# Optimization experiments

Hardware: AMD Instinct MI355X
Metric: run time of the kernel (lower is better)

The kernel has to match this reference:

```python
import jax, jax.numpy as jnp
import numpy as np

SEQ, BATCH, IN_DIM, HID_DIM = 512, 256, 256, 256
NQ = 8
ALPHA = 0.5
MLP_HID = 128


def _linear_init(key, fan_in, fan_out):
    k1, k2 = jax.random.split(key)
    bound = 1.0 / np.sqrt(fan_in)
    W = jax.random.uniform(k1, (fan_in, fan_out), minval=-bound, maxval=bound, dtype=jnp.float32)
    b = jax.random.uniform(k2, (fan_out,), minval=-bound, maxval=bound, dtype=jnp.float32)
    return W, b


def setup_inputs() -> dict:
    key = jax.random.key(0)
    ks = jax.random.split(key, 12)
    cdim = IN_DIM + HID_DIM
    inputs = jax.random.normal(ks[0], (SEQ, BATCH, IN_DIM), dtype=jnp.float32)
    W1, b1 = _linear_init(ks[1], cdim, MLP_HID)
    W2, b2 = _linear_init(ks[2], MLP_HID, NQ * 4)
    Wf, bf = _linear_init(ks[3], cdim, 1)
    Wi, bi = _linear_init(ks[4], cdim, 1)
    Wg, bg = _linear_init(ks[5], cdim, 1)
    Wo, bo = _linear_init(ks[6], cdim, 1)
    rzf = jax.random.normal(ks[7], (NQ,), dtype=jnp.float32)
    rzi = jax.random.normal(ks[8], (NQ,), dtype=jnp.float32)
    rzg = jax.random.normal(ks[9], (NQ,), dtype=jnp.float32)
    rzo = jax.random.normal(ks[10], (NQ,), dtype=jnp.float32)
    return dict(inputs=inputs, W1=W1, b1=b1, W2=W2, b2=b2,
                Wf=Wf, bf=bf, Wi=Wi, bi=bi, Wg=Wg, bg=bg, Wo=Wo, bo=bo,
                rzf=rzf, rzi=rzi, rzg=rzg, rzo=rzo)


def _qgate(theta):
    # Analytic expectations of the RX/RZ/CNOT-chain circuit:
    # <Z_k> = prod_{j<=k} cos(theta_j); rz_params cancel in Z expectations.
    # Returns mean over wires, shape (batch, 1).
    return jnp.mean(jnp.cumprod(jnp.cos(theta), axis=-1), axis=-1, keepdims=True)


def reference(inputs, W1, b1, W2, b2, Wf, bf, Wi, bi, Wg, bg, Wo, bo, rzf, rzi, rzg, rzo):
    batch = inputs.shape[1]
    hx0 = jnp.zeros((batch, HID_DIM), dtype=inputs.dtype)
    cx0 = jnp.zeros((batch, HID_DIM), dtype=inputs.dtype)

    def step(carry, x):
        hx, cx = carry
        combined = jnp.concatenate([x, hx], axis=1)  # (B, in+hid)
        f_c = jax.nn.sigmoid(combined @ Wf + bf)
        i_c = jax.nn.sigmoid(combined @ Wi + bi)
        g_c = jnp.tanh(combined @ Wg + bg)
        o_c = jax.nn.sigmoid(combined @ Wo + bo)
        h1 = jax.nn.relu(combined @ W1 + b1)
        q = h1 @ W2 + b2  # (B, 4*NQ)
        q_f = _qgate(q[:, 0 * NQ:1 * NQ])
        q_i = _qgate(q[:, 1 * NQ:2 * NQ])
        q_g = _qgate(q[:, 2 * NQ:3 * NQ])
        q_o = _qgate(q[:, 3 * NQ:4 * NQ])
        f = (1 - ALPHA) * f_c + ALPHA * jax.nn.sigmoid(q_f)
        i = (1 - ALPHA) * i_c + ALPHA * jax.nn.sigmoid(q_i)
        g = (1 - ALPHA) * g_c + ALPHA * jnp.tanh(q_g)
        o = (1 - ALPHA) * o_c + ALPHA * jax.nn.sigmoid(q_o)
        cx_new = f * cx + i * g
        hx_new = o * jnp.tanh(cx_new)
        return (hx_new, cx_new), hx_new

    (hx, cx), outputs = jax.lax.scan(step, (hx0, cx0), inputs)
    return outputs, (hx, cx)
```

## Files before the change

### kernel.cpp

```cpp
#include <hip/hip_runtime.h>

#define SEQ 512
#define BATCH 256
#define INDIM 256
#define MLP 128
#define M_ROWS (SEQ * BATCH)
#define PRE_STRIDE 136
#define AUX_OFF ((size_t)M_ROWS * PRE_STRIDE)

__global__ __launch_bounds__(256) void prep_kernel(
    const float* __restrict__ W1,
    const float* __restrict__ Wf, const float* __restrict__ Wi,
    const float* __restrict__ Wg, const float* __restrict__ Wo,
    const float* __restrict__ bf, const float* __restrict__ bi,
    const float* __restrict__ bg, const float* __restrict__ bo,
    float* __restrict__ aux) {
  const int tid = threadIdx.x;
  if (tid < 128) {
    float s = 0.f;
    for (int k = 0; k < 256; ++k) s += W1[(size_t)(256 + k) * 128 + tid];
    aux[tid] = s;
  } else if (tid < 132) {
    const int g = tid - 128;
    const float* w = (g == 0) ? Wf : (g == 1) ? Wi : (g == 2) ? Wg : Wo;
    float s = 0.f;
    for (int k = 0; k < 256; ++k) s += w[256 + k];
    aux[128 + g] = s;
  } else if (tid < 136) {
    const int g = tid - 132;
    const float* bp = (g == 0) ? bf : (g == 1) ? bi : (g == 2) ? bg : bo;
    aux[132 + g] = bp[0];
  }
}

#define BK 16
#define LDX 132

__global__ __launch_bounds__(256) void gemm_kernel(
    const float* __restrict__ X,
    const float* __restrict__ W1,
    const float* __restrict__ b1p,
    const float* __restrict__ Wf, const float* __restrict__ Wi,
    const float* __restrict__ Wg, const float* __restrict__ Wo,
    const float* __restrict__ bfp, const float* __restrict__ bip,
    const float* __restrict__ bgp, const float* __restrict__ bop,
    float* __restrict__ PRE) {
  __shared__ __align__(16) float Xs[BK * LDX];
  __shared__ __align__(16) float Ws[BK * LDX];
  __shared__ float Wgs[BK * 4];

  const int tid = threadIdx.x;
  const int blk = blockIdx.x;
  const int tx = tid & 15, ty = tid >> 4;
  const int r_st = tid >> 1, kh = (tid & 1) * 8;
  const int wk = tid >> 4, wn = (tid & 15) * 8;
  const int r2 = tid >> 1, gp = (tid & 1) * 2;

  const size_t rowbase = (size_t)blk * 128;

  float acc[8][8] = {};
  float ga = 0.f, gb = 0.f;

  for (int kc = 0; kc < 256; kc += BK) {
    const float4 xa = *(const float4*)&X[(rowbase + r_st) * 256 + kc + kh];
    const float4 xb = *(const float4*)&X[(rowbase + r_st) * 256 + kc + kh + 4];
    const float4 wa = *(const float4*)&W1[(size_t)(kc + wk) * 128 + wn];
    const float4 wb = *(const float4*)&W1[(size_t)(kc + wk) * 128 + wn + 4];
    float wgv = 0.f;
    if (tid < 64) {
      const int kk = tid >> 2, g = tid & 3;
      const float* w = (g == 0) ? Wf : (g == 1) ? Wi : (g == 2) ? Wg : Wo;
      wgv = w[kc + kk];
    }
    __syncthreads();
    Xs[(kh + 0) * LDX + r_st] = xa.x;
    Xs[(kh + 1) * LDX + r_st] = xa.y;
    Xs[(kh + 2) * LDX + r_st] = xa.z;
    Xs[(kh + 3) * LDX + r_st] = xa.w;
    Xs[(kh + 4) * LDX + r_st] = xb.x;
    Xs[(kh + 5) * LDX + r_st] = xb.y;
    Xs[(kh + 6) * LDX + r_st] = xb.z;
    Xs[(kh + 7) * LDX + r_st] = xb.w;
    *(float4*)&Ws[wk * LDX + wn] = wa;
    *(float4*)&Ws[wk * LDX + wn + 4] = wb;
    if (tid < 64) Wgs[tid] = wgv;
    __syncthreads();

#pragma unroll
    for (int kk = 0; kk < BK; ++kk) {
      const float4 a0 = *(const float4*)&Xs[kk * LDX + ty * 8];
      const float4 a1 = *(const float4*)&Xs[kk * LDX + ty * 8 + 4];
      const float4 c0 = *(const float4*)&Ws[kk * LDX + tx * 8];
      const float4 c1 = *(const float4*)&Ws[kk * LDX + tx * 8 + 4];
      const float av[8] = {a0.x, a0.y, a0.z, a0.w, a1.x, a1.y, a1.z, a1.w};
      const float bv[8] = {c0.x, c0.y, c0.z, c0.w, c1.x, c1.y, c1.z, c1.w};
#pragma unroll
      for (int i = 0; i < 8; ++i)
#pragma unroll
        for (int j = 0; j < 8; ++j)
          acc[i][j] = fmaf(av[i], bv[j], acc[i][j]);
      const float xv = Xs[kk * LDX + r2];
      ga = fmaf(xv, Wgs[kk * 4 + gp], ga);
      gb = fmaf(xv, Wgs[kk * 4 + gp + 1], gb);
    }
  }

  float bias[8];
  {
    const float4 u0 = *(const float4*)&b1p[tx * 8];
    const float4 u1 = *(const float4*)&b1p[tx * 8 + 4];
    bias[0] = u0.x; bias[1] = u0.y; bias[2] = u0.z; bias[3] = u0.w;
    bias[4] = u1.x; bias[5] = u1.y; bias[6] = u1.z; bias[7] = u1.w;
  }
#pragma unroll
  for (int i = 0; i < 8; ++i) {
    const size_t row = rowbase + ty * 8 + i;
    float4 o0, o1;
    o0.x = acc[i][0] + bias[0]; o0.y = acc[i][1] + bias[1];
    o0.z = acc[i][2] + bias[2]; o0.w = acc[i][3] + bias[3];
    o1.x = acc[i][4] + bias[4]; o1.y = acc[i][5] + bias[5];
    o1.z = acc[i][6] + bias[6]; o1.w = acc[i][7] + bias[7];
    *(float4*)&PRE[row * PRE_STRIDE + tx * 8] = o0;
    *(float4*)&PRE[row * PRE_STRIDE + tx * 8 + 4] = o1;
  }
  {
    const float ab = (gp == 0) ? bfp[0] : bgp[0];
    const float bb2 = (gp == 0) ? bip[0] : bop[0];
    float2 og;
    og.x = ga + ab; og.y = gb + bb2;
    *(float2*)&PRE[(rowbase + r2) * PRE_STRIDE + 128 + gp] = og;
  }
}

__device__ __forceinline__ float sigmoid_f(float x) {
  return __fdividef(1.0f, 1.0f + __expf(-x));
}
__device__ __forceinline__ float tanh_f(float x) {
  const float e = __expf(-2.0f * x);
  return __fdividef(1.0f - e, 1.0f + e);
}
__device__ __forceinline__ float readlane_f(float v, int lane) {
  return __int_as_float(__builtin_amdgcn_readlane(__float_as_int(v), lane));
}

__global__ __attribute__((amdgpu_waves_per_eu(1, 1))) __launch_bounds__(64)
void rec_kernel(
    const float* __restrict__ PRE, const float* __restrict__ W2,
    const float* __restrict__ b2, const float* __restrict__ aux,
    float* __restrict__ out) {
  __shared__ __align__(16) float h1s[128];

  const int l = threadIdx.x;
  const int b = blockIdx.x;
  const int m = l & 31, half = l >> 5;
  const int g = m >> 3;
  const int g8 = g * 8;

  float w2r[64];
#pragma unroll
  for (int u = 0; u < 64; ++u) w2r[u] = W2[(size_t)(half * 64 + u) * 32 + m];
  const float4 b2a = *(const float4*)&b2[g8];
  const float4 b2b = *(const float4*)&b2[g8 + 4];
  const float2 s1 = *(const float2*)&aux[2 * l];
  const float4 sg = *(const float4*)&aux[128];

  float h = 0.f, c = 0.f;

  const float* pr0 = PRE + (size_t)b * PRE_STRIDE;
  const size_t ts = (size_t)BATCH * PRE_STRIDE;

  float2 p0 = *(const float2*)(pr0 + 0 * ts + 2 * l);
  float4 g0 = *(const float4*)(pr0 + 0 * ts + 128);
  float2 p1 = *(const float2*)(pr0 + 1 * ts + 2 * l);
  float4 g1 = *(const float4*)(pr0 + 1 * ts + 128);

  const float4* h1p = (const float4*)&h1s[half * 64];

  for (int t = 0; t < SEQ; ++t) {
    const float h10 = fmaxf(fmaf(h, s1.x, p0.x), 0.f);
    const float h11 = fmaxf(fmaf(h, s1.y, p0.y), 0.f);

    ((float2*)h1s)[l] = make_float2(h10, h11);
    asm volatile("" ::: "memory");

    const float zf = fmaf(h, sg.x, g0.x);
    const float zi = fmaf(h, sg.y, g0.y);
    const float zg = fmaf(h, sg.z, g0.z);
    const float zo = fmaf(h, sg.w, g0.w);
    const float cf = sigmoid_f(zf);
    const float ci = sigmoid_f(zi);
    const float cg = tanh_f(zg);
    const float co = sigmoid_f(zo);
    p0 = p1; g0 = g1;
    const int tn = (t + 2 < SEQ) ? (t + 2) : (SEQ - 1);
    p1 = *(const float2*)(pr0 + (size_t)tn * ts + 2 * l);
    g1 = *(const float4*)(pr0 + (size_t)tn * ts + 128);

    float q0 = 0.f, q1 = 0.f, q2 = 0.f, q3 = 0.f;
#pragma unroll
    for (int jj = 0; jj < 16; ++jj) {
      const float4 hv = h1p[jj];
      q0 = fmaf(hv.x, w2r[4 * jj + 0], q0);
      q1 = fmaf(hv.y, w2r[4 * jj + 1], q1);
      q2 = fmaf(hv.z, w2r[4 * jj + 2], q2);
      q3 = fmaf(hv.w, w2r[4 * jj + 3], q3);
    }
    const float part = (q0 + q1) + (q2 + q3);

    const float a0 = __shfl(part, g8 + 0, 64), b0 = __shfl(part, 32 + g8 + 0, 64);
    const float a1 = __shfl(part, g8 + 1, 64), b1 = __shfl(part, 32 + g8 + 1, 64);
    const float a2 = __shfl(part, g8 + 2, 64), b2s = __shfl(part, 32 + g8 + 2, 64);
    const float a3 = __shfl(part, g8 + 3, 64), b3 = __shfl(part, 32 + g8 + 3, 64);
    const float a4 = __shfl(part, g8 + 4, 64), b4 = __shfl(part, 32 + g8 + 4, 64);
    const float a5 = __shfl(part, g8 + 5, 64), b5 = __shfl(part, 32 + g8 + 5, 64);
    const float a6 = __shfl(part, g8 + 6, 64), b6 = __shfl(part, 32 + g8 + 6, 64);
    const float a7 = __shfl(part, g8 + 7, 64), b7 = __shfl(part, 32 + g8 + 7, 64);

    const float e0 = __cosf(a0 + b0 + b2a.x);
    const float e1 = __cosf(a1 + b1 + b2a.y);
    const float e2 = __cosf(a2 + b2s + b2a.z);
    const float e3 = __cosf(a3 + b3 + b2a.w);
    const float e4 = __cosf(a4 + b4 + b2b.x);
    const float e5 = __cosf(a5 + b5 + b2b.y);
    const float e6 = __cosf(a6 + b6 + b2b.z);
    const float e7 = __cosf(a7 + b7 + b2b.w);
    float p = e0, s = e0;
    p *= e1; s += p;
    p *= e2; s += p;
    p *= e3; s += p;
    p *= e4; s += p;
    p *= e5; s += p;
    p *= e6; s += p;
    p *= e7; s += p;
    const float qv = s * 0.125f;

    const float qarg = (g == 2) ? (2.0f * qv) : qv;
    const float qs = sigmoid_f(qarg);
    const float av = (g == 2) ? (2.0f * qs - 1.0f) : qs;

    const float aF = readlane_f(av, 0);
    const float aI = readlane_f(av, 8);
    const float aG = readlane_f(av, 16);
    const float aO = readlane_f(av, 24);

    const float f  = 0.5f * (cf + aF);
    const float ii = 0.5f * (ci + aI);
    const float gg = 0.5f * (cg + aG);
    const float oo = 0.5f * (co + aO);

    c = fmaf(f, c, ii * gg);
    h = oo * tanh_f(c);

    float4 hv4o; hv4o.x = h; hv4o.y = h; hv4o.z = h; hv4o.w = h;
    *(float4*)(out + ((size_t)t * BATCH + b) * 256 + 4 * l) = hv4o;
  }

  float4 hq; hq.x = h; hq.y = h; hq.z = h; hq.w = h;
  float4 cq; cq.x = c; cq.y = c; cq.z = c; cq.w = c;
  *(float4*)(out + (size_t)SEQ * BATCH * 256 + (size_t)b * 256 + 4 * l) = hq;
  *(float4*)(out + (size_t)SEQ * BATCH * 256 + (size_t)BATCH * 256 +
             (size_t)b * 256 + 4 * l) = cq;
}

extern "C" void kernel_launch(void* const* d_in, const int* in_sizes, int n_in,
                              void* d_out, int out_size, void* d_ws,
                              size_t ws_size, hipStream_t stream) {
  const float* X  = (const float*)d_in[0];
  const float* W1 = (const float*)d_in[1];
  const float* b1 = (const float*)d_in[2];
  const float* W2 = (const float*)d_in[3];
  const float* b2 = (const float*)d_in[4];
  const float* Wf = (const float*)d_in[5];
  const float* bf = (const float*)d_in[6];
  const float* Wi = (const float*)d_in[7];
  const float* bi = (const float*)d_in[8];
  const float* Wg = (const float*)d_in[9];
  const float* bg = (const float*)d_in[10];
  const float* Wo = (const float*)d_in[11];
  const float* bo = (const float*)d_in[12];

  float* ws  = (float*)d_ws;
  float* PRE = ws;
  float* aux = ws + AUX_OFF;
  float* out = (float*)d_out;

  prep_kernel<<<1, 256, 0, stream>>>(W1, Wf, Wi, Wg, Wo, bf, bi, bg, bo, aux);
  gemm_kernel<<<M_ROWS / 128, 256, 0, stream>>>(X, W1, b1, Wf, Wi, Wg, Wo,
                                                bf, bi, bg, bo, PRE);
  rec_kernel<<<BATCH, 64, 0, stream>>>(PRE, W2, b2, aux, out);
}
```

Before: 762.1 us.

## Use bf16 MFMA for input projection and interleave two batch rows per recurrent wave

The fp32 SIMT GEMM that projects the inputs onto the MLP and gate weights is replaced by a bf16 MFMA 16x16x32 GEMM. A new prep kernel transposes and converts the weights to bf16, and the activations are rounded to bf16 on load. Separately, the recurrent kernel now processes two batch rows per 64-lane wave, interleaving their independent dependency chains to hide latency while halving the number of workgroups. Using bf16 lowers the precision of the pre-activations, and putting two rows on each wave halves the parallelism across CUs.

```diff
diff --git a/kernel.cpp b/kernel.cpp
--- a/kernel.cpp
+++ b/kernel.cpp
@@ -8,8 +8,16 @@
 #define PRE_STRIDE 136
 #define AUX_OFF ((size_t)M_ROWS * PRE_STRIDE)
 
+typedef __attribute__((ext_vector_type(8))) short short8v;
+typedef __attribute__((ext_vector_type(4))) float f32x4;
+
+__device__ __forceinline__ ushort bf16_rne(float x) {
+  const uint u = __float_as_uint(x);
+  return (ushort)((u + 0x7FFFu + ((u >> 16) & 1u)) >> 16);
+}
+
 __global__ __launch_bounds__(256) void prep_kernel(
-    const float* __restrict__ W1,
+    const float* __restrict__ W1, const float* __restrict__ b1p,
     const float* __restrict__ Wf, const float* __restrict__ Wi,
     const float* __restrict__ Wg, const float* __restrict__ Wo,
     const float* __restrict__ bf, const float* __restrict__ bi,
@@ -26,109 +34,96 @@
     float s = 0.f;
     for (int k = 0; k < 256; ++k) s += w[256 + k];
     aux[128 + g] = s;
-  } else if (tid < 136) {
-    const int g = tid - 132;
-    const float* bp = (g == 0) ? bf : (g == 1) ? bi : (g == 2) ? bg : bo;
-    aux[132 + g] = bp[0];
-  }
-}
-
-#define BK 16
-#define LDX 132
-
-__global__ __launch_bounds__(256) void gemm_kernel(
-    const float* __restrict__ X,
+  }
+  if (tid < 144) {
+    float v;
+    if (tid < 128) v = b1p[tid];
+    else if (tid < 132) {
+      const int g = tid - 128;
+      v = (g == 0) ? bf[0] : (g == 1) ? bi[0] : (g == 2) ? bg[0] : bo[0];
+    } else v = 0.f;
+    aux[160 + tid] = v;
+  }
+}
+
+__global__ __launch_bounds__(256) void prep2_kernel(
     const float* __restrict__ W1,
-    const float* __restrict__ b1p,
     const float* __restrict__ Wf, const float* __restrict__ Wi,
     const float* __restrict__ Wg, const float* __restrict__ Wo,
-    const float* __restrict__ bfp, const float* __restrict__ bip,
-    const float* __restrict__ bgp, const float* __restrict__ bop,
-    float* __restrict__ PRE) {
-  __shared__ __align__(16) float Xs[BK * LDX];
-  __shared__ __align__(16) float Ws[BK * LDX];
-  __shared__ float Wgs[BK * 4];
+    ushort* __restrict__ W1T) {
+  const int n = blockIdx.x;
+  const int k = threadIdx.x;
+  float v;
+  if (n < 128) v = W1[(size_t)k * 128 + n];
+  else if (n < 132) {
+    const int g = n - 128;
+    const float* w = (g == 0) ? Wf : (g == 1) ? Wi : (g == 2) ? Wg : Wo;
+    v = w[k];
+  } else v = 0.f;
+  W1T[(size_t)n * 264 + k] = bf16_rne(v);
+}
+
+__global__ __launch_bounds__(256) void gemm_kernel(
+    const float* __restrict__ X, const ushort* __restrict__ W1T,
+    const float* __restrict__ b1ext, float* __restrict__ PRE) {
+  __shared__ __align__(16) ushort As[64 * 40];
+  __shared__ __align__(16) ushort Bs[144 * 40];
 
   const int tid = threadIdx.x;
-  const int blk = blockIdx.x;
-  const int tx = tid & 15, ty = tid >> 4;
-  const int r_st = tid >> 1, kh = (tid & 1) * 8;
-  const int wk = tid >> 4, wn = (tid & 15) * 8;
-  const int r2 = tid >> 1, gp = (tid & 1) * 2;
-
-  const size_t rowbase = (size_t)blk * 128;
-
-  float acc[8][8] = {};
-  float ga = 0.f, gb = 0.f;
-
-  for (int kc = 0; kc < 256; kc += BK) {
-    const float4 xa = *(const float4*)&X[(rowbase + r_st) * 256 + kc + kh];
-    const float4 xb = *(const float4*)&X[(rowbase + r_st) * 256 + kc + kh + 4];
-    const float4 wa = *(const float4*)&W1[(size_t)(kc + wk) * 128 + wn];
-    const float4 wb = *(const float4*)&W1[(size_t)(kc + wk) * 128 + wn + 4];
-    float wgv = 0.f;
-    if (tid < 64) {
-      const int kk = tid >> 2, g = tid & 3;
-      const float* w = (g == 0) ? Wf : (g == 1) ? Wi : (g == 2) ? Wg : Wo;
-      wgv = w[kc + kk];
-    }
+  const int lane = tid & 63, wave = tid >> 6;
+  const int m = lane & 15, quad = lane >> 4;
+  const int arow = tid >> 2, aseg = tid & 3;
+  const size_t rowbase = (size_t)blockIdx.x * 64;
+
+  const f32x4 zero = {0.f, 0.f, 0.f, 0.f};
+  f32x4 acc[9];
+#pragma unroll
+  for (int nt = 0; nt < 9; ++nt) acc[nt] = zero;
+
+  for (int kc = 0; kc < 256; kc += 32) {
     __syncthreads();
-    Xs[(kh + 0) * LDX + r_st] = xa.x;
-    Xs[(kh + 1) * LDX + r_st] = xa.y;
-    Xs[(kh + 2) * LDX + r_st] = xa.z;
-    Xs[(kh + 3) * LDX + r_st] = xa.w;
-    Xs[(kh + 4) * LDX + r_st] = xb.x;
-    Xs[(kh + 5) * LDX + r_st] = xb.y;
-    Xs[(kh + 6) * LDX + r_st] = xb.z;
-    Xs[(kh + 7) * LDX + r_st] = xb.w;
-    *(float4*)&Ws[wk * LDX + wn] = wa;
-    *(float4*)&Ws[wk * LDX + wn + 4] = wb;
-    if (tid < 64) Wgs[tid] = wgv;
+    {
+      const float* src = &X[(rowbase + arow) * 256 + kc + aseg * 8];
+      const float4 v0 = *(const float4*)src;
+      const float4 v1 = *(const float4*)(src + 4);
+      uint4 w;
+      w.x = (uint)bf16_rne(v0.x) | ((uint)bf16_rne(v0.y) << 16);
+      w.y = (uint)bf16_rne(v0.z) | ((uint)bf16_rne(v0.w) << 16);
+      w.z = (uint)bf16_rne(v1.x) | ((uint)bf16_rne(v1.y) << 16);
+      w.w = (uint)bf16_rne(v1.z) | ((uint)bf16_rne(v1.w) << 16);
+      *(uint4*)&As[arow * 40 + aseg * 8] = w;
+    }
+    if (tid < 144) {
+      const ushort* src = &W1T[(size_t)tid * 264 + kc];
+      const uint4 b0 = *(const uint4*)(src + 0);
+      const uint4 b1v = *(const uint4*)(src + 8);
+      const uint4 b2v = *(const uint4*)(src + 16);
+      const uint4 b3v = *(const uint4*)(src + 24);
+      *(uint4*)&Bs[tid * 40 + 0] = b0;
+      *(uint4*)&Bs[tid * 40 + 8] = b1v;
+      *(uint4*)&Bs[tid * 40 + 16] = b2v;
+      *(uint4*)&Bs[tid * 40 + 24] = b3v;
+    }
     __syncthreads();
 
-#pragma unroll
-    for (int kk = 0; kk < BK; ++kk) {
-      const float4 a0 = *(const float4*)&Xs[kk * LDX + ty * 8];
-      const float4 a1 = *(const float4*)&Xs[kk * LDX + ty * 8 + 4];
-      const float4 c0 = *(const float4*)&Ws[kk * LDX + tx * 8];
-      const float4 c1 = *(const float4*)&Ws[kk * LDX + tx * 8 + 4];
-      const float av[8] = {a0.x, a0.y, a0.z, a0.w, a1.x, a1.y, a1.z, a1.w};
-      const float bv[8] = {c0.x, c0.y, c0.z, c0.w, c1.x, c1.y, c1.z, c1.w};
-#pragma unroll
-      for (int i = 0; i < 8; ++i)
-#pragma unroll
-        for (int j = 0; j < 8; ++j)
-          acc[i][j] = fmaf(av[i], bv[j], acc[i][j]);
-      const float xv = Xs[kk * LDX + r2];
-      ga = fmaf(xv, Wgs[kk * 4 + gp], ga);
-      gb = fmaf(xv, Wgs[kk * 4 + gp + 1], gb);
-    }
-  }
-
-  float bias[8];
-  {
-    const float4 u0 = *(const float4*)&b1p[tx * 8];
-    const float4 u1 = *(const float4*)&b1p[tx * 8 + 4];
-    bias[0] = u0.x; bias[1] = u0.y; bias[2] = u0.z; bias[3] = u0.w;
-    bias[4] = u1.x; bias[5] = u1.y; bias[6] = u1.z; bias[7] = u1.w;
-  }
-#pragma unroll
-  for (int i = 0; i < 8; ++i) {
-    const size_t row = rowbase + ty * 8 + i;
-    float4 o0, o1;
-    o0.x = acc[i][0] + bias[0]; o0.y = acc[i][1] + bias[1];
-    o0.z = acc[i][2] + bias[2]; o0.w = acc[i][3] + bias[3];
-    o1.x = acc[i][4] + bias[4]; o1.y = acc[i][5] + bias[5];
-    o1.z = acc[i][6] + bias[6]; o1.w = acc[i][7] + bias[7];
-    *(float4*)&PRE[row * PRE_STRIDE + tx * 8] = o0;
-    *(float4*)&PRE[row * PRE_STRIDE + tx * 8 + 4] = o1;
-  }
-  {
-    const float ab = (gp == 0) ? bfp[0] : bgp[0];
-    const float bb2 = (gp == 0) ? bip[0] : bop[0];
-    float2 og;
-    og.x = ga + ab; og.y = gb + bb2;
-    *(float2*)&PRE[(rowbase + r2) * PRE_STRIDE + 128 + gp] = og;
+    const short8v af = *(const short8v*)&As[(wave * 16 + m) * 40 + quad * 8];
+#pragma unroll
+    for (int nt = 0; nt < 9; ++nt) {
+      const short8v bfr = *(const short8v*)&Bs[(nt * 16 + m) * 40 + quad * 8];
+      acc[nt] = __builtin_amdgcn_mfma_f32_16x16x32_bf16(af, bfr, acc[nt], 0, 0, 0);
+    }
+  }
+
+#pragma unroll
+  for (int nt = 0; nt < 9; ++nt) {
+    const int col = nt * 16 + m;
+    if (col < 132) {
+      const float bias = b1ext[col];
+      const size_t r0 = rowbase + wave * 16 + quad * 4;
+#pragma unroll
+      for (int reg = 0; reg < 4; ++reg)
+        PRE[(r0 + reg) * PRE_STRIDE + col] = acc[nt][reg] + bias;
+    }
   }
 }
 
@@ -148,13 +143,13 @@
     const float* __restrict__ PRE, const float* __restrict__ W2,
     const float* __restrict__ b2, const float* __restrict__ aux,
     float* __restrict__ out) {
-  __shared__ __align__(16) float h1s[128];
+  __shared__ __align__(16) float h1sA[128];
+  __shared__ __align__(16) float h1sB[128];
 
   const int l = threadIdx.x;
-  const int b = blockIdx.x;
   const int m = l & 31, half = l >> 5;
-  const int g = m >> 3;
-  const int g8 = g * 8;
+  const int g = m >> 3, g8 = g * 8;
+  const int bA = blockIdx.x * 2, bB = bA + 1;
 
   float w2r[64];
 #pragma unroll
@@ -164,102 +159,160 @@
   const float2 s1 = *(const float2*)&aux[2 * l];
   const float4 sg = *(const float4*)&aux[128];
 
-  float h = 0.f, c = 0.f;
-
-  const float* pr0 = PRE + (size_t)b * PRE_STRIDE;
+  float hA = 0.f, cA = 0.f, hB = 0.f, cB = 0.f;
+
+  const float* prA = PRE + (size_t)bA * PRE_STRIDE;
+  const float* prB = PRE + (size_t)bB * PRE_STRIDE;
   const size_t ts = (size_t)BATCH * PRE_STRIDE;
 
-  float2 p0 = *(const float2*)(pr0 + 0 * ts + 2 * l);
-  float4 g0 = *(const float4*)(pr0 + 0 * ts + 128);
-  float2 p1 = *(const float2*)(pr0 + 1 * ts + 2 * l);
-  float4 g1 = *(const float4*)(pr0 + 1 * ts + 128);
-
-  const float4* h1p = (const float4*)&h1s[half * 64];
+  float2 pA0 = *(const float2*)(prA + 0 * ts + 2 * l);
+  float4 gA0 = *(const float4*)(prA + 0 * ts + 128);
+  float2 pA1 = *(const float2*)(prA + 1 * ts + 2 * l);
+  float4 gA1 = *(const float4*)(prA + 1 * ts + 128);
+  float2 pB0 = *(const float2*)(prB + 0 * ts + 2 * l);
+  float4 gB0 = *(const float4*)(prB + 0 * ts + 128);
+  float2 pB1 = *(const float2*)(prB + 1 * ts + 2 * l);
+  float4 gB1 = *(const float4*)(prB + 1 * ts + 128);
+
+  const float4* hpA = (const float4*)&h1sA[half * 64];
+  const float4* hpB = (const float4*)&h1sB[half * 64];
 
   for (int t = 0; t < SEQ; ++t) {
-    const float h10 = fmaxf(fmaf(h, s1.x, p0.x), 0.f);
-    const float h11 = fmaxf(fmaf(h, s1.y, p0.y), 0.f);
-
-    ((float2*)h1s)[l] = make_float2(h10, h11);
+    const int tn = (t + 2 < SEQ) ? (t + 2) : (SEQ - 1);
+
+    const float h10A = fmaxf(fmaf(hA, s1.x, pA0.x), 0.f);
+    const float h11A = fmaxf(fmaf(hA, s1.y, pA0.y), 0.f);
+    ((float2*)h1sA)[l] = make_float2(h10A, h11A);
+    const float cfA = sigmoid_f(fmaf(hA, sg.x, gA0.x));
+    const float ciA = sigmoid_f(fmaf(hA, sg.y, gA0.y));
+    const float cgA = tanh_f(fmaf(hA, sg.z, gA0.z));
+    const float coA = sigmoid_f(fmaf(hA, sg.w, gA0.w));
+    pA0 = pA1; gA0 = gA1;
+    pA1 = *(const float2*)(prA + (size_t)tn * ts + 2 * l);
+    gA1 = *(const float4*)(prA + (size_t)tn * ts + 128);
+
+    const float h10B = fmaxf(fmaf(hB, s1.x, pB0.x), 0.f);
+    const float h11B = fmaxf(fmaf(hB, s1.y, pB0.y), 0.f);
+    ((float2*)h1sB)[l] = make_float2(h10B, h11B);
+    const float cfB = sigmoid_f(fmaf(hB, sg.x, gB0.x));
+    const float ciB = sigmoid_f(fmaf(hB, sg.y, gB0.y));
+    const float cgB = tanh_f(fmaf(hB, sg.z, gB0.z));
+    const float coB = sigmoid_f(fmaf(hB, sg.w, gB0.w));
+    pB0 = pB1; gB0 = gB1;
+    pB1 = *(const float2*)(prB + (size_t)tn * ts + 2 * l);
+    gB1 = *(const float4*)(prB + (size_t)tn * ts + 128);
+
     asm volatile("" ::: "memory");
 
-    const float zf = fmaf(h, sg.x, g0.x);
-    const float zi = fmaf(h, sg.y, g0.y);
-    const float zg = fmaf(h, sg.z, g0.z);
-    const float zo = fmaf(h, sg.w, g0.w);
-    const float cf = sigmoid_f(zf);
-    const float ci = sigmoid_f(zi);
-    const float cg = tanh_f(zg);
-    const float co = sigmoid_f(zo);
-    p0 = p1; g0 = g1;
-    const int tn = (t + 2 < SEQ) ? (t + 2) : (SEQ - 1);
-    p1 = *(const float2*)(pr0 + (size_t)tn * ts + 2 * l);
-    g1 = *(const float4*)(pr0 + (size_t)tn * ts + 128);
-
-    float q0 = 0.f, q1 = 0.f, q2 = 0.f, q3 = 0.f;
+    float qa0 = 0.f, qa1 = 0.f, qa2 = 0.f, qa3 = 0.f;
 #pragma unroll
     for (int jj = 0; jj < 16; ++jj) {
-      const float4 hv = h1p[jj];
-      q0 = fmaf(hv.x, w2r[4 * jj + 0], q0);
-      q1 = fmaf(hv.y, w2r[4 * jj + 1], q1);
-      q2 = fmaf(hv.z, w2r[4 * jj + 2], q2);
-      q3 = fmaf(hv.w, w2r[4 * jj + 3], q3);
-    }
-    const float part = (q0 + q1) + (q2 + q3);
-
-    const float a0 = __shfl(part, g8 + 0, 64), b0 = __shfl(part, 32 + g8 + 0, 64);
-    const float a1 = __shfl(part, g8 + 1, 64), b1 = __shfl(part, 32 + g8 + 1, 64);
-    const float a2 = __shfl(part, g8 + 2, 64), b2s = __shfl(part, 32 + g8 + 2, 64);
-    const float a3 = __shfl(part, g8 + 3, 64), b3 = __shfl(part, 32 + g8 + 3, 64);
-    const float a4 = __shfl(part, g8 + 4, 64), b4 = __shfl(part, 32 + g8 + 4, 64);
-    const float a5 = __shfl(part, g8 + 5, 64), b5 = __shfl(part, 32 + g8 + 5, 64);
-    const float a6 = __shfl(part, g8 + 6, 64), b6 = __shfl(part, 32 + g8 + 6, 64);
-    const float a7 = __shfl(part, g8 + 7, 64), b7 = __shfl(part, 32 + g8 + 7, 64);
-
-    const float e0 = __cosf(a0 + b0 + b2a.x);
-    const float e1 = __cosf(a1 + b1 + b2a.y);
-    const float e2 = __cosf(a2 + b2s + b2a.z);
-    const float e3 = __cosf(a3 + b3 + b2a.w);
-    const float e4 = __cosf(a4 + b4 + b2b.x);
-    const float e5 = __cosf(a5 + b5 + b2b.y);
-    const float e6 = __cosf(a6 + b6 + b2b.z);
-    const float e7 = __cosf(a7 + b7 + b2b.w);
-    float p = e0, s = e0;
-    p *= e1; s += p;
-    p *= e2; s += p;
-    p *= e3; s += p;
-    p *= e4; s += p;
-    p *= e5; s += p;
-    p *= e6; s += p;
-    p *= e7; s += p;
-    const float qv = s * 0.125f;
-
-    const float qarg = (g == 2) ? (2.0f * qv) : qv;
-    const float qs = sigmoid_f(qarg);
-    const float av = (g == 2) ? (2.0f * qs - 1.0f) : qs;
-
-    const float aF = readlane_f(av, 0);
-    const float aI = readlane_f(av, 8);
-    const float aG = readlane_f(av, 16);
-    const float aO = readlane_f(av, 24);
-
-    const float f  = 0.5f * (cf + aF);
-    const float ii = 0.5f * (ci + aI);
-    const float gg = 0.5f * (cg + aG);
-    const float oo = 0.5f * (co + aO);
-
-    c = fmaf(f, c, ii * gg);
-    h = oo * tanh_f(c);
-
-    float4 hv4o; hv4o.x = h; hv4o.y = h; hv4o.z = h; hv4o.w = h;
-    *(float4*)(out + ((size_t)t * BATCH + b) * 256 + 4 * l) = hv4o;
-  }
-
-  float4 hq; hq.x = h; hq.y = h; hq.z = h; hq.w = h;
-  float4 cq; cq.x = c; cq.y = c; cq.z = c; cq.w = c;
-  *(float4*)(out + (size_t)SEQ * BATCH * 256 + (size_t)b * 256 + 4 * l) = hq;
+      const float4 hv = hpA[jj];
+      qa0 = fmaf(hv.x, w2r[4 * jj + 0], qa0);
+      qa1 = fmaf(hv.y, w2r[4 * jj + 1], qa1);
+      qa2 = fmaf(hv.z, w2r[4 * jj + 2], qa2);
+      qa3 = fmaf(hv.w, w2r[4 * jj + 3], qa3);
+    }
+    const float partA = (qa0 + qa1) + (qa2 + qa3);
+
+    float qb0 = 0.f, qb1 = 0.f, qb2 = 0.f, qb3 = 0.f;
+#pragma unroll
+    for (int jj = 0; jj < 16; ++jj) {
+      const float4 hv = hpB[jj];
+      qb0 = fmaf(hv.x, w2r[4 * jj + 0], qb0);
+      qb1 = fmaf(hv.y, w2r[4 * jj + 1], qb1);
+      qb2 = fmaf(hv.z, w2r[4 * jj + 2], qb2);
+      qb3 = fmaf(hv.w, w2r[4 * jj + 3], qb3);
+    }
+    const float partB = (qb0 + qb1) + (qb2 + qb3);
+
+    {
+      const float a0 = __shfl(partA, g8 + 0, 64), b0 = __shfl(partA, 32 + g8 + 0, 64);
+      const float a1 = __shfl(partA, g8 + 1, 64), b1 = __shfl(partA, 32 + g8 + 1, 64);
+      const float a2 = __shfl(partA, g8 + 2, 64), b2v = __shfl(partA, 32 + g8 + 2, 64);
+      const float a3 = __shfl(partA, g8 + 3, 64), b3 = __shfl(partA, 32 + g8 + 3, 64);
+      const float a4 = __shfl(partA, g8 + 4, 64), b4 = __shfl(partA, 32 + g8 + 4, 64);
+      const float a5 = __shfl(partA, g8 + 5, 64), b5 = __shfl(partA, 32 + g8 + 5, 64);
+      const float a6 = __shfl(partA, g8 + 6, 64), b6 = __shfl(partA, 32 + g8 + 6, 64);
+      const float a7 = __shfl(partA, g8 + 7, 64), b7 = __shfl(partA, 32 + g8 + 7, 64);
+      const float e0 = __cosf(a0 + b0 + b2a.x);
+      const float e1 = __cosf(a1 + b1 + b2a.y);
+      const float e2 = __cosf(a2 + b2v + b2a.z);
+      const float e3 = __cosf(a3 + b3 + b2a.w);
+      const float e4 = __cosf(a4 + b4 + b2b.x);
+      const float e5 = __cosf(a5 + b5 + b2b.y);
+      const float e6 = __cosf(a6 + b6 + b2b.z);
+      const float e7 = __cosf(a7 + b7 + b2b.w);
+      float p = e0, s = e0;
+      p *= e1; s += p; p *= e2; s += p; p *= e3; s += p;
+      p *= e4; s += p; p *= e5; s += p; p *= e6; s += p; p *= e7; s += p;
+      const float qv = s * 0.125f;
+      const float qarg = (g == 2) ? (2.0f * qv) : qv;
+      const float qs = sigmoid_f(qarg);
+      const float av = (g == 2) ? (2.0f * qs - 1.0f) : qs;
+      const float aF = readlane_f(av, 0);
+      const float aI = readlane_f(av, 8);
+      const float aG = readlane_f(av, 16);
+      const float aO = readlane_f(av, 24);
+      const float f  = 0.5f * (cfA + aF);
+      const float ii = 0.5f * (ciA + aI);
+      const float gg = 0.5f * (cgA + aG);
+      const float oo = 0.5f * (coA + aO);
+      cA = fmaf(f, cA, ii * gg);
+      hA = oo * tanh_f(cA);
+      float4 hv4o; hv4o.x = hA; hv4o.y = hA; hv4o.z = hA; hv4o.w = hA;
+      *(float4*)(out + ((size_t)t * BATCH + bA) * 256 + 4 * l) = hv4o;
+    }
+    {
+      const float a0 = __shfl(partB, g8 + 0, 64), b0 = __shfl(partB, 32 + g8 + 0, 64);
+      const float a1 = __shfl(partB, g8 + 1, 64), b1 = __shfl(partB, 32 + g8 + 1, 64);
+      const float a2 = __shfl(partB, g8 + 2, 64), b2v = __shfl(partB, 32 + g8 + 2, 64);
+      const float a3 = __shfl(partB, g8 + 3, 64), b3 = __shfl(partB, 32 + g8 + 3, 64);
+      const float a4 = __shfl(partB, g8 + 4, 64), b4 = __shfl(partB, 32 + g8 + 4, 64);
+      const float a5 = __shfl(partB, g8 + 5, 64), b5 = __shfl(partB, 32 + g8 + 5, 64);
+      const float a6 = __shfl(partB, g8 + 6, 64), b6 = __shfl(partB, 32 + g8 + 6, 64);
+      const float a7 = __shfl(partB, g8 + 7, 64), b7 = __shfl(partB, 32 + g8 + 7, 64);
+      const float e0 = __cosf(a0 + b0 + b2a.x);
+      const float e1 = __cosf(a1 + b1 + b2a.y);
+      const float e2 = __cosf(a2 + b2v + b2a.z);
+      const float e3 = __cosf(a3 + b3 + b2a.w);
+      const float e4 = __cosf(a4 + b4 + b2b.x);
+      const float e5 = __cosf(a5 + b5 + b2b.y);
+      const float e6 = __cosf(a6 + b6 + b2b.z);
+      const float e7 = __cosf(a7 + b7 + b2b.w);
+      float p = e0, s = e0;
+      p *= e1; s += p; p *= e2; s += p; p *= e3; s += p;
+      p *= e4; s += p; p *= e5; s += p; p *= e6; s += p; p *= e7; s += p;
+      const float qv = s * 0.125f;
+      const float qarg = (g == 2) ? (2.0f * qv) : qv;
+      const float qs = sigmoid_f(qarg);
+      const float av = (g == 2) ? (2.0f * qs - 1.0f) : qs;
+      const float aF = readlane_f(av, 0);
+      const float aI = readlane_f(av, 8);
+      const float aG = readlane_f(av, 16);
+      const float aO = readlane_f(av, 24);
+      const float f  = 0.5f * (cfB + aF);
+      const float ii = 0.5f * (ciB + aI);
+      const float gg = 0.5f * (cgB + aG);
+      const float oo = 0.5f * (coB + aO);
+      cB = fmaf(f, cB, ii * gg);
+      hB = oo * tanh_f(cB);
+      float4 hv4o; hv4o.x = hB; hv4o.y = hB; hv4o.z = hB; hv4o.w = hB;
+      *(float4*)(out + ((size_t)t * BATCH + bB) * 256 + 4 * l) = hv4o;
+    }
+  }
+
+  float4 hq, cq;
+  hq.x = hA; hq.y = hA; hq.z = hA; hq.w = hA;
+  cq.x = cA; cq.y = cA; cq.z = cA; cq.w = cA;
+  *(float4*)(out + (size_t)SEQ * BATCH * 256 + (size_t)bA * 256 + 4 * l) = hq;
   *(float4*)(out + (size_t)SEQ * BATCH * 256 + (size_t)BATCH * 256 +
-             (size_t)b * 256 + 4 * l) = cq;
+             (size_t)bA * 256 + 4 * l) = cq;
+  hq.x = hB; hq.y = hB; hq.z = hB; hq.w = hB;
+  cq.x = cB; cq.y = cB; cq.z = cB; cq.w = cB;
+  *(float4*)(out + (size_t)SEQ * BATCH * 256 + (size_t)bB * 256 + 4 * l) = hq;
+  *(float4*)(out + (size_t)SEQ * BATCH * 256 + (size_t)BATCH * 256 +
+             (size_t)bB * 256 + 4 * l) = cq;
 }
 
 extern "C" void kernel_launch(void* const* d_in, const int* in_sizes, int n_in,
@@ -279,13 +332,16 @@
   const float* Wo = (const float*)d_in[11];
   const float* bo = (const float*)d_in[12];
 
-  float* ws  = (float*)d_ws;
-  float* PRE = ws;
-  float* aux = ws + AUX_OFF;
-  float* out = (float*)d_out;
-
-  prep_kernel<<<1, 256, 0, stream>>>(W1, Wf, Wi, Wg, Wo, bf, bi, bg, bo, aux);
-  gemm_kernel<<<M_ROWS / 128, 256, 0, stream>>>(X, W1, b1, Wf, Wi, Wg, Wo,
-                                                bf, bi, bg, bo, PRE);
-  rec_kernel<<<BATCH, 64, 0, stream>>>(PRE, W2, b2, aux, out);
-}
+  float* ws   = (float*)d_ws;
+  float* PRE  = ws;
+  float* aux  = ws + AUX_OFF;
+  float* b1ext = aux + 160;
+  ushort* W1T = (ushort*)(aux + 320);
+  float* out  = (float*)d_out;
+
+  prep_kernel<<<1, 256, 0, stream>>>(W1, b1, Wf, Wi, Wg, Wo,
+                                     bf, bi, bg, bo, aux);
+  prep2_kernel<<<144, 256, 0, stream>>>(W1, Wf, Wi, Wg, Wo, W1T);
+  gemm_kernel<<<M_ROWS / 64, 256, 0, stream>>>(X, W1T, b1ext, PRE);
+  rec_kernel<<<BATCH / 2, 64, 0, stream>>>(PRE, W2, b2, aux, out);
+}
```

Result: slower. 988.0 us (+29.6%).
